# Kernel tuning notes

Measured on AMD Instinct MI355X. Metric: run time of the kernel, lower is better.

The kernel has to match this reference:

```python
import jax, jax.numpy as jnp
import numpy as np

HID, NH = 2048, 16
QLR, KVLR = 1536, 512
DR, DN, DQK, DV = 64, 128, 192, 128
S = 2048
EPS = 1e-06


def rmsnorm(x, w, eps=EPS):
    return x * jax.lax.rsqrt(jnp.mean(x * x, axis=-1, keepdims=True) + eps) * w


def rope_interleave(x, cos, sin):
    # x: [B,H,S,D]; cos/sin: [B,S,D] (unsqueezed to head dim 1)
    b, h, s, d = x.shape
    # DeepSeek-V3 interleave: (d//2, 2) -> transpose -> flatten
    x = x.reshape(b, h, s, d // 2, 2).swapaxes(3, 4).reshape(b, h, s, d)
    c = cos[:, None, :, :]
    sn = sin[:, None, :, :]
    x1, x2 = x[..., : d // 2], x[..., d // 2:]
    rot = jnp.concatenate([-x2, x1], axis=-1)
    return x * c + rot * sn


def setup_inputs() -> dict:
    key = jax.random.key(0)
    ks = jax.random.split(key, 8)
    hidden_states = jax.random.normal(ks[0], (1, S, HID), dtype=jnp.float32)
    # real RoPE tables for the 64-dim rope part
    inv_freq = 1.0 / (10000.0 ** (np.arange(0, DR, 2, dtype=np.float32) / DR))
    pos = np.arange(S, dtype=np.float32)
    freqs = pos[:, None] * inv_freq[None, :]          # [S, DR/2]
    emb = np.concatenate([freqs, freqs], axis=-1)     # [S, DR]
    cos = jnp.asarray(np.cos(emb), dtype=jnp.float32)[None]
    sin = jnp.asarray(np.sin(emb), dtype=jnp.float32)[None]
    w = 0.02
    wq_a = jax.random.normal(ks[1], (QLR, HID), dtype=jnp.float32) * w
    q_a_ln_w = jnp.ones((QLR,), dtype=jnp.float32)
    wq_b = jax.random.normal(ks[2], (NH * DQK, QLR), dtype=jnp.float32) * w
    wkv_a = jax.random.normal(ks[3], (KVLR + DR, HID), dtype=jnp.float32) * w
    kv_a_ln_w = jnp.ones((KVLR,), dtype=jnp.float32)
    wkv_b = jax.random.normal(ks[4], (NH * (DN + DV), KVLR), dtype=jnp.float32) * w
    wo = jax.random.normal(ks[5], (HID, NH * DV), dtype=jnp.float32) * w
    cu_seqlens = jnp.array([0, S // 2, S], dtype=jnp.int32)  # two packed docs
    return {"hidden_states": hidden_states, "cos": cos, "sin": sin,
            "wq_a": wq_a, "q_a_ln_w": q_a_ln_w, "wq_b": wq_b,
            "wkv_a": wkv_a, "kv_a_ln_w": kv_a_ln_w, "wkv_b": wkv_b,
            "wo": wo, "cu_seqlens": cu_seqlens, "max_seqlen": S // 2}


def reference(hidden_states, cos, sin, wq_a, q_a_ln_w, wq_b, wkv_a, kv_a_ln_w,
              wkv_b, wo, cu_seqlens, max_seqlen):
    B, s, _ = hidden_states.shape
    # LoRA-compressed Q: q_a -> RMSNorm -> q_b
    q = rmsnorm(hidden_states @ wq_a.T, q_a_ln_w) @ wq_b.T       # [B,S,NH*DQK]
    q = q.reshape(B, s, NH, DQK).transpose(0, 2, 1, 3)           # [B,NH,S,DQK]
    q_pass, q_rot = q[..., :DN], q[..., DN:]
    # compressed KV with MQA rope part
    ckv = hidden_states @ wkv_a.T                                 # [B,S,KVLR+DR]
    kv_c, k_rot = ckv[..., :KVLR], ckv[..., KVLR:]
    kv = rmsnorm(kv_c, kv_a_ln_w) @ wkv_b.T                       # [B,S,NH*(DN+DV)]
    kv = kv.reshape(B, s, NH, DN + DV).transpose(0, 2, 1, 3)      # [B,NH,S,DN+DV]
    k_pass, v = kv[..., :DN], kv[..., DN:]
    k_rot = k_rot[:, None, :, :]                                  # [B,1,S,DR]
    q_rot = rope_interleave(q_rot, cos, sin)
    k_rot = rope_interleave(k_rot, cos, sin)
    k_rot = jnp.broadcast_to(k_rot, (B, NH, s, DR))
    qf = jnp.concatenate([q_pass, q_rot], axis=-1)                # [B,NH,S,DQK]
    kf = jnp.concatenate([k_pass, k_rot], axis=-1)                # [B,NH,S,DQK]
    # varlen causal attention: block-diagonal per document + causal
    pos = jnp.arange(s)
    seg = jnp.searchsorted(cu_seqlens[1:], pos, side='right')
    mask = (seg[:, None] == seg[None, :]) & (pos[:, None] >= pos[None, :])
    scale = DQK ** -0.5  # flash default: 1/sqrt(q head dim) (v padded to DQK)
    scores = jnp.einsum('bhqd,bhkd->bhqk', qf, kf) * scale
    scores = jnp.where(mask[None, None], scores, jnp.finfo(scores.dtype).min)
    attn = jax.nn.softmax(scores, axis=-1)
    out = jnp.einsum('bhqk,bhkd->bhqd', attn, v)                  # [B,NH,S,DV]
    out = out.transpose(0, 2, 1, 3).reshape(B, s, NH * DV)
    return out @ wo.T
```

## Files before the change

### kernel.cpp

```cpp
#include <hip/hip_runtime.h>

typedef unsigned short u16;
typedef __attribute__((ext_vector_type(8))) short bf16x8;
typedef __attribute__((ext_vector_type(4))) float f32x4;

#define HID 2048
#define NH 16
#define QLR 1536
#define KVLR 512
#define DR 64
#define DN 128
#define DQK 192
#define DV 128
#define SEQ 2048
#define NKVA 2176
#define SCALE 0.07216878364870323f
#define SCL2 0.1041164359699839f
#define THR2 11.541560327111707f

static __device__ __forceinline__ u16 f2bf(float f) {
  unsigned v = __builtin_bit_cast(unsigned, f);
  v = v + 0x7fffu + ((v >> 16) & 1u);
  return (u16)(v >> 16);
}
static __device__ __forceinline__ float bf2f(u16 u) {
  unsigned v = ((unsigned)u) << 16;
  return __builtin_bit_cast(float, v);
}

#define GLOAD16(gp, lp)                                                        \
  __builtin_amdgcn_global_load_lds(                                            \
      (const __attribute__((address_space(1))) void*)(gp),                     \
      (__attribute__((address_space(3))) void*)(lp), 16, 0, 0)

__global__ void k_convert_all(const float* __restrict__ hs, const float* __restrict__ wq_a,
                              const float* __restrict__ wkv_a, const float* __restrict__ wqb,
                              const float* __restrict__ wkvb, const float* __restrict__ wo,
                              u16* __restrict__ hs_bf, u16* __restrict__ wqkva,
                              u16* __restrict__ wqb_bf, u16* __restrict__ wkvb_bf,
                              u16* __restrict__ wo_bf) {
  const long NQ = 4915200;
  long q = (long)blockIdx.x * blockDim.x + threadIdx.x;
  const long stride = (long)gridDim.x * blockDim.x;
  for (; q < NQ; q += stride) {
    const float* src;
    u16* dst;
    long li;
    bool zero = false;
    if (q < 1048576)        { src = hs;   dst = hs_bf;                      li = q; }
    else if (q < 1835008)   { src = wq_a; dst = wqkva;                      li = q - 1048576; }
    else if (q < 2162688)   { li = q - 1835008; src = wkv_a; dst = wqkva + (size_t)QLR * HID;
                              zero = (li >= 294912); }
    else if (q < 3342336)   { src = wqb;  dst = wqb_bf;                     li = q - 2162688; }
    else if (q < 3866624)   { src = wkvb; dst = wkvb_bf;                    li = q - 3342336; }
    else                    { src = wo;   dst = wo_bf;                      li = q - 3866624; }
    u16 o0 = 0, o1 = 0, o2 = 0, o3 = 0;
    if (!zero) {
      const float4 f = *(const float4*)(src + li * 4);
      o0 = f2bf(f.x); o1 = f2bf(f.y); o2 = f2bf(f.z); o3 = f2bf(f.w);
    }
    u16* d = dst + li * 4;
    d[0] = o0; d[1] = o1; d[2] = o2; d[3] = o3;
  }
}

__global__ void k_rmsnorm2(const float* __restrict__ qkva, const float* __restrict__ qw,
                           const float* __restrict__ kvw, u16* __restrict__ q_ln,
                           u16* __restrict__ kv_ln) {
  const int row = blockIdx.x;
  const int which = blockIdx.y;
  const int t = threadIdx.x;
  const int cols = which ? KVLR : QLR;
  const float inv_cols = which ? (1.0f / KVLR) : (1.0f / QLR);
  const float* x = qkva + (size_t)row * NKVA + (which ? QLR : 0);
  const float* w = which ? kvw : qw;
  u16* Y = (which ? kv_ln : q_ln) + (size_t)row * cols;
  float ss = 0.f;
  for (int i = t * 4; i < cols; i += 1024) {
    float4 v = *(const float4*)(x + i);
    ss += v.x * v.x + v.y * v.y + v.z * v.z + v.w * v.w;
  }
#pragma unroll
  for (int m = 1; m < 64; m <<= 1) ss += __shfl_xor(ss, m, 64);
  __shared__ float red[4];
  if ((t & 63) == 0) red[t >> 6] = ss;
  __syncthreads();
  float tot = red[0] + red[1] + red[2] + red[3];
  float r = rsqrtf(tot * inv_cols + 1e-6f);
  for (int i = t * 4; i < cols; i += 1024) {
    float4 v = *(const float4*)(x + i);
    float4 g = *(const float4*)(w + i);
    u16* y = Y + i;
    y[0] = f2bf(v.x * r * g.x);
    y[1] = f2bf(v.y * r * g.y);
    y[2] = f2bf(v.z * r * g.z);
    y[3] = f2bf(v.w * r * g.w);
  }
}

template <int WN, int NBUF>
__global__ __launch_bounds__(512) void k_gemm_nt8(
    const u16* __restrict__ A, const u16* __restrict__ B, void* __restrict__ Cout,
    int M, int N, int K, int mode) {
  constexpr int BN = WN * 64;
  constexpr int NST = 2 + WN;
  __shared__ __align__(16) u16 As[NBUF][128 * 64];
  __shared__ __align__(16) u16 Bs[NBUF][BN * 64];
  const int t = threadIdx.x;
  const int lane = t & 63;
  const int w = t >> 6, wr = w >> 2, wc = w & 3;
  const int lm = lane & 15, lg = lane >> 4;

  const int nwg = gridDim.x * gridDim.y;
  int bid = blockIdx.y * gridDim.x + blockIdx.x;
  if ((nwg & 7) == 0) bid = (bid & 7) * (nwg >> 3) + (bid >> 3);
  const int bm = bid % gridDim.y;
  const int bn = bid / gridDim.y;

  const u16* aT = A + (size_t)bm * 128 * K;
  const u16* bT = B + (size_t)bn * BN * K;

#define STAGE8(buf, kt_)                                                       \
  do {                                                                         \
    _Pragma("unroll") for (int i = 0; i < 2; ++i) {                            \
      const int g = t + i * 512, row = g >> 3, slot = (g & 7) ^ (row & 7);     \
      GLOAD16(aT + (size_t)row * K + slot * 8 + (kt_), (u16*)As[buf] + g * 8); \
    }                                                                          \
    _Pragma("unroll") for (int i = 0; i < WN; ++i) {                           \
      const int g = t + i * 512, row = g >> 3, slot = (g & 7) ^ (row & 7);     \
      GLOAD16(bT + (size_t)row * K + slot * 8 + (kt_), (u16*)Bs[buf] + g * 8); \
    }                                                                          \
  } while (0)

  f32x4 acc[4][WN] = {};
  const int nk = K >> 6;
#pragma unroll
  for (int b = 0; b < NBUF; ++b)
    if (b < nk) STAGE8(b, b << 6);
  int bt = 0;
  for (int kt = 0; kt < nk; ++kt) {
    const int rem = nk - 1 - kt;
    if constexpr (NBUF == 3) {
      if (rem >= 2)      asm volatile("s_waitcnt vmcnt(%0)" :: "i"(2 * NST) : "memory");
      else if (rem == 1) asm volatile("s_waitcnt vmcnt(%0)" :: "i"(NST) : "memory");
      else               asm volatile("s_waitcnt vmcnt(0)" ::: "memory");
    } else {
      if (rem >= 1)      asm volatile("s_waitcnt vmcnt(%0)" :: "i"(NST) : "memory");
      else               asm volatile("s_waitcnt vmcnt(0)" ::: "memory");
    }
    __builtin_amdgcn_s_barrier();
    __builtin_amdgcn_sched_barrier(0);
    bf16x8 af[2][4], bfr[2][WN];
#pragma unroll
    for (int kk = 0; kk < 2; ++kk) {
#pragma unroll
      for (int i = 0; i < 4; ++i) {
        const int row_ = wr * 64 + i * 16 + lm;
        af[kk][i] = *(const bf16x8*)(As[bt] + row_ * 64 +
                                     ((((kk << 2) | lg) ^ (row_ & 7)) << 3));
      }
#pragma unroll
      for (int j = 0; j < WN; ++j) {
        const int row_ = wc * (WN * 16) + j * 16 + lm;
        bfr[kk][j] = *(const bf16x8*)(Bs[bt] + row_ * 64 +
                                      ((((kk << 2) | lg) ^ (row_ & 7)) << 3));
      }
    }
    asm volatile("s_waitcnt lgkmcnt(0)" ::: "memory");
    __builtin_amdgcn_sched_barrier(0);
    __builtin_amdgcn_s_barrier();
    __builtin_amdgcn_sched_barrier(0);
    if (kt + NBUF < nk) STAGE8(bt, (kt + NBUF) << 6);
    __builtin_amdgcn_s_setprio(1);
#pragma unroll
    for (int kk = 0; kk < 2; ++kk)
#pragma unroll
      for (int i = 0; i < 4; ++i)
#pragma unroll
        for (int j = 0; j < WN; ++j)
          acc[i][j] = __builtin_amdgcn_mfma_f32_16x16x32_bf16(af[kk][i], bfr[kk][j],
                                                              acc[i][j], 0, 0, 0);
    __builtin_amdgcn_s_setprio(0);
    bt = (bt == NBUF - 1) ? 0 : bt + 1;
  }
#undef STAGE8

  const int row0 = bm * 128 + wr * 64 + lg * 4;
  const int col0 = bn * BN + wc * (WN * 16) + lm;
  if (mode == 1) {
    u16* C = (u16*)Cout;
#pragma unroll
    for (int i = 0; i < 4; ++i)
#pragma unroll
      for (int r = 0; r < 4; ++r) {
        u16* crow = C + (size_t)(row0 + i * 16 + r) * N + col0;
#pragma unroll
        for (int j = 0; j < WN; ++j) crow[j * 16] = f2bf(acc[i][j][r]);
      }
  } else {
    float* C = (float*)Cout;
#pragma unroll
    for (int i = 0; i < 4; ++i)
#pragma unroll
      for (int r = 0; r < 4; ++r) {
        float* crow = C + (size_t)(row0 + i * 16 + r) * N + col0;
#pragma unroll
        for (int j = 0; j < WN; ++j) crow[j * 16] = acc[i][j][r];
      }
  }
}

__global__ __launch_bounds__(256) void k_mk_all(
    const u16* __restrict__ qfull, const u16* __restrict__ kvfull,
    const float* __restrict__ krot, int krot_stride,
    const float* __restrict__ cosb, const float* __restrict__ sinb,
    u16* __restrict__ qf, u16* __restrict__ kf, u16* __restrict__ vt) {
  __shared__ u16 vts[128][66];
  const int s0 = blockIdx.x * 64, h = blockIdx.y, t = threadIdx.x;
#pragma unroll
  for (int i = 0; i < 8; ++i) {
    const int g = t + i * 256, row = g >> 5, slot = g & 31;
    const u16* src = kvfull + (size_t)(s0 + row) * (NH * 256) + h * 256 + slot * 8;
    bf16x8 v = *(const bf16x8*)src;
    if (slot < 16) {
      *(bf16x8*)(kf + ((size_t)h * SEQ + s0 + row) * DQK + slot * 8) = v;
    } else {
      const int d = (slot - 16) * 8;
#pragma unroll
      for (int e = 0; e < 8; ++e) vts[d + e][row] = (u16)v[e];
    }
  }
#pragma unroll
  for (int i = 0; i < 8; ++i) {
    const int g = t + i * 256, row = g >> 5, c = g & 31;
    const size_t kb = (size_t)(s0 + row) * krot_stride + 2 * c;
    float a = krot[kb];
    float b = krot[kb + 1];
    float cc = cosb[(size_t)(s0 + row) * DR + c];
    float sn = sinb[(size_t)(s0 + row) * DR + c];
    u16* kd = kf + ((size_t)h * SEQ + s0 + row) * DQK;
    kd[DN + c] = f2bf(a * cc - b * sn);
    kd[DN + 32 + c] = f2bf(b * cc + a * sn);
  }
  __syncthreads();
#pragma unroll
  for (int i = 0; i < 4; ++i) {
    const int g = t + i * 256, d = g >> 3, slot = g & 7;
    bf16x8 v;
#pragma unroll
    for (int e = 0; e < 8; ++e) v[e] = (short)vts[d][slot * 8 + e];
    *(bf16x8*)(vt + ((size_t)h * DV + d) * SEQ + s0 + slot * 8) = v;
  }
#pragma unroll
  for (int i = 0; i < 4; ++i) {
    const int g = t + i * 256, row = g >> 4, vc = g & 15;
    const u16* src = qfull + (size_t)(s0 + row) * (NH * DQK) + h * DQK + vc * 8;
    bf16x8 v = *(const bf16x8*)src;
    bf16x8 o;
#pragma unroll
    for (int e = 0; e < 8; ++e) o[e] = (short)f2bf(bf2f((u16)v[e]) * SCL2);
    *(bf16x8*)(qf + ((size_t)h * SEQ + s0 + row) * DQK + vc * 8) = o;
  }
#pragma unroll
  for (int i = 0; i < 8; ++i) {
    const int g = t + i * 256, row = g >> 5, c = g & 31;
    const u16* src = qfull + (size_t)(s0 + row) * (NH * DQK) + h * DQK;
    float a = bf2f(src[DN + 2 * c]);
    float b = bf2f(src[DN + 2 * c + 1]);
    float cc = cosb[(size_t)(s0 + row) * DR + c];
    float sn = sinb[(size_t)(s0 + row) * DR + c];
    u16* qd = qf + ((size_t)h * SEQ + s0 + row) * DQK;
    qd[DN + c] = f2bf((a * cc - b * sn) * SCL2);
    qd[DN + 32 + c] = f2bf((b * cc + a * sn) * SCL2);
  }
}

__global__ __launch_bounds__(256) void k_attn(
    const u16* __restrict__ qf, const u16* __restrict__ kf, const u16* __restrict__ vt,
    u16* __restrict__ attn_out, float* __restrict__ O_part, float* __restrict__ mlbuf) {
  __shared__ __align__(16) u16 Ks[2][32 * 192];
  __shared__ __align__(16) u16 Vs[2][128 * 32];
  __shared__ __align__(16) u16 p_lds[4][16][32];

  static const signed char TJ[24] = {15,15,7,14,14,13,13,6,12,12,11,11,5,
                                     10,10,9,9,4,8,8,3,2,1,0};
  static const signed char CK[24] = {0,1,2,0,1,0,1,2,0,1,0,1,2,
                                     0,1,0,1,2,0,1,2,2,2,2};

  const int t = threadIdx.x, lane = t & 63, w = t >> 6;
  const int lm = lane & 15, lg = lane >> 4;
  const int bid = blockIdx.x;
  const int x = bid & 7, rr = bid >> 3;
  const int hh = rr & 1, idx = rr >> 1;
  const int seg = idx & 1, slot = idx >> 1;
  const int tj = TJ[slot], ck = CK[slot];
  const int h = x * 2 + hh;
  const int tile_row0 = seg * 1024 + tj * 64;
  const int k_begin = seg * 1024;
  const int n_all = 2 * tj + 2;
  const int kt_lo = (ck == 1) ? (tj + 1) : 0;
  const int kt_hi = (ck == 0) ? (tj + 1) : n_all;
  const int n_kt = kt_hi - kt_lo;

  const int lo_row = tile_row0 + w * 16;
  bf16x8 qfr[6];
  {
    const u16* qp = qf + ((size_t)h * SEQ + (lo_row + lm)) * DQK + lg * 8;
#pragma unroll
    for (int c = 0; c < 6; ++c) qfr[c] = *(const bf16x8*)(qp + c * 32);
  }
  int qrow[4];
#pragma unroll
  for (int r = 0; r < 4; ++r) qrow[r] = lo_row + lg * 4 + r;

  float m_r[4], l_loc[4];
#pragma unroll
  for (int r = 0; r < 4; ++r) { m_r[r] = -3.0e4f; l_loc[r] = 0.f; }
  f32x4 oacc[8] = {};
  bf16x8 pa, vv[8];

#define STAGEA(buf, kt_)                                                       \
  do {                                                                         \
    const int k0_ = k_begin + (kt_) * 32;                                      \
    _Pragma("unroll") for (int p = 0; p < 3; ++p) {                            \
      const int id = p * 256 + t;                                              \
      const int row = id / 24, colL = id - row * 24;                           \
      const u16* g = kf + ((size_t)h * SEQ + k0_ + row) * DQK +                \
                     ((colL ^ (row & 7)) * 8);                                 \
      GLOAD16(g, (u16*)Ks[buf] + id * 8);                                      \
    }                                                                          \
    _Pragma("unroll") for (int p = 0; p < 2; ++p) {                            \
      const int id = p * 256 + t;                                              \
      const int row = id >> 2, colL = id & 3;                                  \
      const u16* g = vt + ((size_t)h * DV + row) * SEQ + k0_ +                 \
                     ((colL ^ (row & 3)) * 8);                                 \
      GLOAD16(g, (u16*)Vs[buf] + id * 8);                                      \
    }                                                                          \
  } while (0)

#define COMPUTE1(buf, kt_)                                                     \
  do {                                                                         \
    const int k0_ = k_begin + (kt_) * 32;                                      \
    f32x4 sc[2] = {};                                                          \
    __builtin_amdgcn_s_setprio(1);                                             \
    _Pragma("unroll") for (int n0_ = 0; n0_ < 2; ++n0_)                        \
        _Pragma("unroll") for (int c_ = 0; c_ < 6; ++c_) {                     \
      const int row_ = n0_ * 16 + lm, cc_ = c_ * 4 + lg;                       \
      bf16x8 kfr = *(const bf16x8*)(Ks[buf] + row_ * 192 +                     \
                                    ((cc_ ^ (row_ & 7)) * 8));                 \
      sc[n0_] = __builtin_amdgcn_mfma_f32_16x16x32_bf16(qfr[c_], kfr,          \
                                                        sc[n0_], 0, 0, 0);     \
    }                                                                          \
    __builtin_amdgcn_s_setprio(0);                                             \
    _Pragma("unroll") for (int nd = 0; nd < 8; ++nd) {                         \
      const int row_ = nd * 16 + lm;                                           \
      vv[nd] = *(const bf16x8*)(Vs[buf] + row_ * 32 +                          \
                                ((lg ^ (row_ & 3)) * 8));                      \
    }                                                                          \
    float s0a[4], s1a[4];                                                      \
    float over = -1e30f;                                                       \
    if (lo_row >= k0_ + 31) {                                                  \
      _Pragma("unroll") for (int r = 0; r < 4; ++r) {                          \
        s0a[r] = sc[0][r];                                                     \
        s1a[r] = sc[1][r];                                                     \
        over = fmaxf(over, fmaxf(s0a[r], s1a[r]) - m_r[r]);                    \
      }                                                                        \
    } else {                                                                   \
      const int kc0 = k0_ + lm, kc1 = k0_ + 16 + lm;                           \
      _Pragma("unroll") for (int r = 0; r < 4; ++r) {                          \
        s0a[r] = (kc0 <= qrow[r]) ? sc[0][r] : -1e30f;                         \
        s1a[r] = (kc1 <= qrow[r]) ? sc[1][r] : -1e30f;                         \
        over = fmaxf(over, fmaxf(s0a[r], s1a[r]) - m_r[r]);                    \
      }                                                                        \
    }                                                                          \
    if (__any(over > THR2)) {                                                  \
      _Pragma("unroll") for (int r = 0; r < 4; ++r) {                          \
        float mx = fmaxf(s0a[r], s1a[r]);                                      \
        _Pragma("unroll") for (int md = 1; md < 16; md <<= 1)                  \
            mx = fmaxf(mx, __shfl_xor(mx, md, 64));                            \
        float mnew = fmaxf(m_r[r], mx);                                        \
        float alpha = exp2f(m_r[r] - mnew);                                    \
        m_r[r] = mnew;                                                         \
        l_loc[r] *= alpha;                                                     \
        _Pragma("unroll") for (int nd = 0; nd < 8; ++nd) oacc[nd][r] *= alpha; \
      }                                                                        \
    }                                                                          \
    _Pragma("unroll") for (int r = 0; r < 4; ++r) {                            \
      float p0 = exp2f(s0a[r] - m_r[r]);                                       \
      float p1 = exp2f(s1a[r] - m_r[r]);                                       \
      l_loc[r] += p0 + p1;                                                     \
      p_lds[w][lg * 4 + r][lm] = f2bf(p0);                                     \
      p_lds[w][lg * 4 + r][16 + lm] = f2bf(p1);                                \
    }                                                                          \
    asm volatile("s_waitcnt lgkmcnt(0)" ::: "memory");                         \
    __builtin_amdgcn_sched_barrier(0);                                         \
    pa = *(const bf16x8*)(&p_lds[w][lm][lg * 8]);                              \
  } while (0)

  STAGEA(0, kt_lo);
  STAGEA(1, kt_lo + 1);
  for (int i = 0; i < n_kt; ++i) {
    const int kt = kt_lo + i;
    if (i + 1 < n_kt) asm volatile("s_waitcnt vmcnt(5)" ::: "memory");
    else              asm volatile("s_waitcnt vmcnt(0)" ::: "memory");
    __builtin_amdgcn_s_barrier();
    __builtin_amdgcn_sched_barrier(0);
    COMPUTE1(i & 1, kt);
    asm volatile("s_waitcnt lgkmcnt(0)" ::: "memory");
    __builtin_amdgcn_sched_barrier(0);
    __builtin_amdgcn_s_barrier();
    __builtin_amdgcn_sched_barrier(0);
    if (i + 2 < n_kt) STAGEA(i & 1, kt + 2);
    __builtin_amdgcn_s_setprio(1);
#pragma unroll
    for (int nd = 0; nd < 8; ++nd)
      oacc[nd] = __builtin_amdgcn_mfma_f32_16x16x32_bf16(pa, vv[nd], oacc[nd], 0, 0, 0);
    __builtin_amdgcn_s_setprio(0);
  }
#undef STAGEA
#undef COMPUTE1

  float l_row[4];
#pragma unroll
  for (int r = 0; r < 4; ++r) {
    float lt = l_loc[r];
#pragma unroll
    for (int md = 1; md < 16; md <<= 1) lt += __shfl_xor(lt, md, 64);
    l_row[r] = lt;
  }

  if (ck == 2) {
#pragma unroll
    for (int r = 0; r < 4; ++r) {
      float inv = 1.0f / l_row[r];
#pragma unroll
      for (int nd = 0; nd < 8; ++nd)
        attn_out[(size_t)qrow[r] * (NH * DV) + h * DV + nd * 16 + lm] =
            f2bf(oacc[nd][r] * inv);
    }
  } else {
    const int part = (((tj - 8) * 2 + seg) * 16 + h) * 2 + ck;
    float* op = O_part + (size_t)part * 8192;
#pragma unroll
    for (int r = 0; r < 4; ++r) {
      const int rw = w * 16 + lg * 4 + r;
#pragma unroll
      for (int nd = 0; nd < 8; ++nd)
        op[rw * 128 + nd * 16 + lm] = oacc[nd][r];
      if (lm == 0) {
        mlbuf[part * 128 + rw] = m_r[r];
        mlbuf[part * 128 + 64 + rw] = l_row[r];
      }
    }
  }
}

__global__ __launch_bounds__(256) void k_merge(const float* __restrict__ O_part,
                                               const float* __restrict__ mlbuf,
                                               u16* __restrict__ attn_out) {
  const int b = blockIdx.x;
  const int h = b & 15, z = b >> 4;
  const int tj = 8 + (z >> 1), seg = z & 1;
  const int p0 = (((tj - 8) * 2 + seg) * 16 + h) * 2;
  const int p1 = p0 + 1;
  const int t = threadIdx.x;
  const int row = t >> 2, cg = t & 3;

  const float m0 = mlbuf[p0 * 128 + row], l0 = mlbuf[p0 * 128 + 64 + row];
  const float m1 = mlbuf[p1 * 128 + row], l1 = mlbuf[p1 * 128 + 64 + row];
  const float M = fmaxf(m0, m1);
  const float w0 = exp2f(m0 - M), w1 = exp2f(m1 - M);
  const float inv = 1.0f / (w0 * l0 + w1 * l1);
  const float a0 = w0 * inv, a1 = w1 * inv;

  const int qrow = seg * 1024 + tj * 64 + row;
  const float* o0 = O_part + (size_t)p0 * 8192 + row * 128 + cg * 32;
  const float* o1 = O_part + (size_t)p1 * 8192 + row * 128 + cg * 32;
  u16* dst = attn_out + (size_t)qrow * (NH * DV) + h * DV + cg * 32;
#pragma unroll
  for (int e = 0; e < 32; e += 4) {
    const float4 u = *(const float4*)(o0 + e);
    const float4 v = *(const float4*)(o1 + e);
    dst[e]     = f2bf(a0 * u.x + a1 * v.x);
    dst[e + 1] = f2bf(a0 * u.y + a1 * v.y);
    dst[e + 2] = f2bf(a0 * u.z + a1 * v.z);
    dst[e + 3] = f2bf(a0 * u.w + a1 * v.w);
  }
}

extern "C" void kernel_launch(void* const* d_in, const int* in_sizes, int n_in,
                              void* d_out, int out_size, void* d_ws, size_t ws_size,
                              hipStream_t stream) {
  const float* hs = (const float*)d_in[0];
  const float* cosb = (const float*)d_in[1];
  const float* sinb = (const float*)d_in[2];
  const float* wq_a = (const float*)d_in[3];
  const float* q_a_ln_w = (const float*)d_in[4];
  const float* wq_b = (const float*)d_in[5];
  const float* wkv_a = (const float*)d_in[6];
  const float* kv_a_ln_w = (const float*)d_in[7];
  const float* wkv_b = (const float*)d_in[8];
  const float* wo = (const float*)d_in[9];

  char* ws = (char*)d_ws;
  size_t off = 0;
  auto take = [&](size_t bytes) {
    size_t o = off;
    off += (bytes + 255) & ~(size_t)255;
    return o;
  };
  u16* hs_bf = (u16*)(ws + take((size_t)SEQ * HID * 2));
  u16* wqkva = (u16*)(ws + take((size_t)NKVA * HID * 2));
  u16* wqb = (u16*)(ws + take((size_t)(NH * DQK) * QLR * 2));
  u16* wkvb = (u16*)(ws + take((size_t)(NH * 256) * KVLR * 2));
  u16* wo_bf = (u16*)(ws + take((size_t)HID * (NH * DV) * 2));
  float* qkva = (float*)(ws + take((size_t)SEQ * NKVA * 4));
  u16* q_ln = (u16*)(ws + take((size_t)SEQ * QLR * 2));
  u16* kv_ln = (u16*)(ws + take((size_t)SEQ * KVLR * 2));
  u16* qfull = (u16*)(ws + take((size_t)SEQ * NH * DQK * 2));
  u16* kvfull = (u16*)(ws + take((size_t)SEQ * NH * 256 * 2));
  u16* qf = (u16*)(ws + take((size_t)NH * SEQ * DQK * 2));
  u16* kf = (u16*)(ws + take((size_t)NH * SEQ * DQK * 2));
  u16* vt = (u16*)(ws + take((size_t)NH * DV * SEQ * 2));
  u16* attn = (u16*)(ws + take((size_t)SEQ * NH * DV * 2));
  if (off > ws_size) return;
  float* O_part = (float*)kvfull;
  float* mlbuf = (float*)qfull;

  k_convert_all<<<2048, 256, 0, stream>>>(hs, wq_a, wkv_a, wq_b, wkv_b, wo,
                                          hs_bf, wqkva, wqb, wkvb, wo_bf);

  dim3 g1(NKVA / 128, SEQ / 128);
  k_gemm_nt8<2, 2><<<g1, 512, 0, stream>>>(hs_bf, wqkva, qkva, SEQ, NKVA, HID, 0);

  k_rmsnorm2<<<dim3(SEQ, 2), 256, 0, stream>>>(qkva, q_a_ln_w, kv_a_ln_w, q_ln, kv_ln);

  dim3 g2(NH * DQK / 192, SEQ / 128);
  k_gemm_nt8<3, 2><<<g2, 512, 0, stream>>>(q_ln, wqb, qfull, SEQ, NH * DQK, QLR, 1);
  dim3 g3(NH * 256 / 256, SEQ / 128);
  k_gemm_nt8<4, 2><<<g3, 512, 0, stream>>>(kv_ln, wkvb, kvfull, SEQ, NH * 256, KVLR, 1);

  k_mk_all<<<dim3(SEQ / 64, NH), 256, 0, stream>>>(qfull, kvfull, qkva + (QLR + KVLR),
                                                   NKVA, cosb, sinb, qf, kf, vt);

  k_attn<<<768, 256, 0, stream>>>(qf, kf, vt, attn, O_part, mlbuf);
  k_merge<<<256, 256, 0, stream>>>(O_part, mlbuf, attn);

  dim3 g4(HID / 128, SEQ / 128);
  k_gemm_nt8<2, 2><<<g4, 512, 0, stream>>>(attn, wo_bf, d_out, SEQ, HID, NH * DV, 0);
}
```

Before: 183.5 us.

## Fuse Q RoPE/scale and K/V split-transpose into GEMM epilogues

```diff
diff --git a/kernel.cpp b/kernel.cpp
--- a/kernel.cpp
+++ b/kernel.cpp
@@ -98,14 +98,16 @@
   }
 }
 
-template <int WN, int NBUF>
+template <int WN, int NBUF, int MODE>
 __global__ __launch_bounds__(512) void k_gemm_nt8(
     const u16* __restrict__ A, const u16* __restrict__ B, void* __restrict__ Cout,
-    int M, int N, int K, int mode) {
+    int M, int N, int K, const float* __restrict__ cosb, const float* __restrict__ sinb,
+    u16* __restrict__ out_a, u16* __restrict__ out_b) {
   constexpr int BN = WN * 64;
   constexpr int NST = 2 + WN;
   __shared__ __align__(16) u16 As[NBUF][128 * 64];
   __shared__ __align__(16) u16 Bs[NBUF][BN * 64];
+  __shared__ __align__(16) u16 vts[MODE == 3 ? 128 * 130 : 2];
   const int t = threadIdx.x;
   const int lane = t & 63;
   const int w = t >> 6, wr = w >> 2, wc = w & 3;
@@ -187,7 +189,7 @@
 
   const int row0 = bm * 128 + wr * 64 + lg * 4;
   const int col0 = bn * BN + wc * (WN * 16) + lm;
-  if (mode == 1) {
+  if constexpr (MODE == 1) {
     u16* C = (u16*)Cout;
 #pragma unroll
     for (int i = 0; i < 4; ++i)
@@ -197,7 +199,7 @@
 #pragma unroll
         for (int j = 0; j < WN; ++j) crow[j * 16] = f2bf(acc[i][j][r]);
       }
-  } else {
+  } else if constexpr (MODE == 0) {
     float* C = (float*)Cout;
 #pragma unroll
     for (int i = 0; i < 4; ++i)
@@ -207,72 +209,80 @@
 #pragma unroll
         for (int j = 0; j < WN; ++j) crow[j * 16] = acc[i][j][r];
       }
-  }
-}
-
-__global__ __launch_bounds__(256) void k_mk_all(
-    const u16* __restrict__ qfull, const u16* __restrict__ kvfull,
-    const float* __restrict__ krot, int krot_stride,
-    const float* __restrict__ cosb, const float* __restrict__ sinb,
-    u16* __restrict__ qf, u16* __restrict__ kf, u16* __restrict__ vt) {
-  __shared__ u16 vts[128][66];
-  const int s0 = blockIdx.x * 64, h = blockIdx.y, t = threadIdx.x;
-#pragma unroll
-  for (int i = 0; i < 8; ++i) {
-    const int g = t + i * 256, row = g >> 5, slot = g & 31;
-    const u16* src = kvfull + (size_t)(s0 + row) * (NH * 256) + h * 256 + slot * 8;
-    bf16x8 v = *(const bf16x8*)src;
-    if (slot < 16) {
-      *(bf16x8*)(kf + ((size_t)h * SEQ + s0 + row) * DQK + slot * 8) = v;
-    } else {
-      const int d = (slot - 16) * 8;
-#pragma unroll
-      for (int e = 0; e < 8; ++e) vts[d + e][row] = (u16)v[e];
+  } else if constexpr (MODE == 2) {
+    const int h = bn;
+#pragma unroll
+    for (int i = 0; i < 4; ++i)
+#pragma unroll
+      for (int r = 0; r < 4; ++r) {
+        const int s = row0 + i * 16 + r;
+        u16* qrow = out_a + ((size_t)h * SEQ + s) * DQK;
+#pragma unroll
+        for (int j = 0; j < WN; ++j) {
+          const int c = wc * 48 + j * 16 + lm;
+          float val = acc[i][j][r];
+          float partner = __shfl_xor(val, 1, 64);
+          if (c < 128) {
+            qrow[c] = f2bf(val * SCL2);
+          } else {
+            const int u = c - 128, p = u >> 1, od = u & 1;
+            float cv = cosb[(size_t)s * DR + p];
+            float sv = sinb[(size_t)s * DR + p];
+            float o = od ? (val * cv + partner * sv) : (val * cv - partner * sv);
+            qrow[128 + od * 32 + p] = f2bf(o * SCL2);
+          }
+        }
+      }
+  } else {
+    const int h = bn;
+    const int sl0 = wr * 64 + lg * 4;
+#pragma unroll
+    for (int i = 0; i < 4; ++i)
+#pragma unroll
+      for (int r = 0; r < 4; ++r) {
+        const int s = row0 + i * 16 + r;
+        const int sl = sl0 + i * 16 + r;
+#pragma unroll
+        for (int j = 0; j < WN; ++j) {
+          const int c = wc * 64 + j * 16 + lm;
+          const u16 bv = f2bf(acc[i][j][r]);
+          if (c < 128) out_a[((size_t)h * SEQ + s) * DQK + c] = bv;
+          else vts[(c - 128) * 130 + sl] = bv;
+        }
+      }
+    __syncthreads();
+    const int d = t >> 2, q4 = t & 3;
+#pragma unroll
+    for (int sub = 0; sub < 4; ++sub) {
+      bf16x8 v;
+#pragma unroll
+      for (int e = 0; e < 8; ++e) v[e] = (short)vts[d * 130 + q4 * 32 + sub * 8 + e];
+      *(bf16x8*)(out_b + ((size_t)h * DV + d) * SEQ + bm * 128 + q4 * 32 + sub * 8) = v;
     }
   }
-#pragma unroll
-  for (int i = 0; i < 8; ++i) {
-    const int g = t + i * 256, row = g >> 5, c = g & 31;
-    const size_t kb = (size_t)(s0 + row) * krot_stride + 2 * c;
-    float a = krot[kb];
-    float b = krot[kb + 1];
-    float cc = cosb[(size_t)(s0 + row) * DR + c];
-    float sn = sinb[(size_t)(s0 + row) * DR + c];
-    u16* kd = kf + ((size_t)h * SEQ + s0 + row) * DQK;
-    kd[DN + c] = f2bf(a * cc - b * sn);
-    kd[DN + 32 + c] = f2bf(b * cc + a * sn);
-  }
-  __syncthreads();
-#pragma unroll
-  for (int i = 0; i < 4; ++i) {
-    const int g = t + i * 256, d = g >> 3, slot = g & 7;
-    bf16x8 v;
-#pragma unroll
-    for (int e = 0; e < 8; ++e) v[e] = (short)vts[d][slot * 8 + e];
-    *(bf16x8*)(vt + ((size_t)h * DV + d) * SEQ + s0 + slot * 8) = v;
-  }
-#pragma unroll
-  for (int i = 0; i < 4; ++i) {
-    const int g = t + i * 256, row = g >> 4, vc = g & 15;
-    const u16* src = qfull + (size_t)(s0 + row) * (NH * DQK) + h * DQK + vc * 8;
-    bf16x8 v = *(const bf16x8*)src;
-    bf16x8 o;
-#pragma unroll
-    for (int e = 0; e < 8; ++e) o[e] = (short)f2bf(bf2f((u16)v[e]) * SCL2);
-    *(bf16x8*)(qf + ((size_t)h * SEQ + s0 + row) * DQK + vc * 8) = o;
-  }
-#pragma unroll
-  for (int i = 0; i < 8; ++i) {
-    const int g = t + i * 256, row = g >> 5, c = g & 31;
-    const u16* src = qfull + (size_t)(s0 + row) * (NH * DQK) + h * DQK;
-    float a = bf2f(src[DN + 2 * c]);
-    float b = bf2f(src[DN + 2 * c + 1]);
-    float cc = cosb[(size_t)(s0 + row) * DR + c];
-    float sn = sinb[(size_t)(s0 + row) * DR + c];
-    u16* qd = qf + ((size_t)h * SEQ + s0 + row) * DQK;
-    qd[DN + c] = f2bf((a * cc - b * sn) * SCL2);
-    qd[DN + 32 + c] = f2bf((b * cc + a * sn) * SCL2);
-  }
+}
+
+__global__ __launch_bounds__(256) void k_rope_k(
+    const float* __restrict__ krot, int stride, const float* __restrict__ cosb,
+    const float* __restrict__ sinb, u16* __restrict__ kf) {
+  const int s0 = blockIdx.x * 32;
+  const int t = threadIdx.x;
+  const int row = t >> 3, c8 = t & 7;
+  const int s = s0 + row;
+  const int half = c8 >> 2, p0 = (c8 & 3) * 8;
+  bf16x8 v;
+#pragma unroll
+  for (int e = 0; e < 8; ++e) {
+    const int p = p0 + e;
+    float a = krot[(size_t)s * stride + 2 * p];
+    float b = krot[(size_t)s * stride + 2 * p + 1];
+    float cv = cosb[(size_t)s * DR + p];
+    float sv = sinb[(size_t)s * DR + p];
+    v[e] = (short)f2bf(half ? (b * cv + a * sv) : (a * cv - b * sv));
+  }
+#pragma unroll
+  for (int h = 0; h < NH; ++h)
+    *(bf16x8*)(kf + ((size_t)h * SEQ + s) * DQK + 128 + half * 32 + p0) = v;
 }
 
 __global__ __launch_bounds__(256) void k_attn(
@@ -517,35 +527,36 @@
   float* qkva = (float*)(ws + take((size_t)SEQ * NKVA * 4));
   u16* q_ln = (u16*)(ws + take((size_t)SEQ * QLR * 2));
   u16* kv_ln = (u16*)(ws + take((size_t)SEQ * KVLR * 2));
-  u16* qfull = (u16*)(ws + take((size_t)SEQ * NH * DQK * 2));
-  u16* kvfull = (u16*)(ws + take((size_t)SEQ * NH * 256 * 2));
   u16* qf = (u16*)(ws + take((size_t)NH * SEQ * DQK * 2));
   u16* kf = (u16*)(ws + take((size_t)NH * SEQ * DQK * 2));
   u16* vt = (u16*)(ws + take((size_t)NH * DV * SEQ * 2));
   u16* attn = (u16*)(ws + take((size_t)SEQ * NH * DV * 2));
+  float* O_part = (float*)(ws + take((size_t)512 * 8192 * 4));
+  float* mlbuf = (float*)(ws + take((size_t)512 * 128 * 4));
   if (off > ws_size) return;
-  float* O_part = (float*)kvfull;
-  float* mlbuf = (float*)qfull;
 
   k_convert_all<<<2048, 256, 0, stream>>>(hs, wq_a, wkv_a, wq_b, wkv_b, wo,
                                           hs_bf, wqkva, wqb, wkvb, wo_bf);
 
   dim3 g1(NKVA / 128, SEQ / 128);
-  k_gemm_nt8<2, 2><<<g1, 512, 0, stream>>>(hs_bf, wqkva, qkva, SEQ, NKVA, HID, 0);
+  k_gemm_nt8<2, 2, 0><<<g1, 512, 0, stream>>>(hs_bf, wqkva, qkva, SEQ, NKVA, HID,
+                                              nullptr, nullptr, nullptr, nullptr);
 
   k_rmsnorm2<<<dim3(SEQ, 2), 256, 0, stream>>>(qkva, q_a_ln_w, kv_a_ln_w, q_ln, kv_ln);
 
+  k_rope_k<<<SEQ / 32, 256, 0, stream>>>(qkva + (QLR + KVLR), NKVA, cosb, sinb, kf);
+
   dim3 g2(NH * DQK / 192, SEQ / 128);
-  k_gemm_nt8<3, 2><<<g2, 512, 0, stream>>>(q_ln, wqb, qfull, SEQ, NH * DQK, QLR, 1);
+  k_gemm_nt8<3, 2, 2><<<g2, 512, 0, stream>>>(q_ln, wqb, nullptr, SEQ, NH * DQK, QLR,
+                                              cosb, sinb, qf, nullptr);
   dim3 g3(NH * 256 / 256, SEQ / 128);
-  k_gemm_nt8<4, 2><<<g3, 512, 0, stream>>>(kv_ln, wkvb, kvfull, SEQ, NH * 256, KVLR, 1);
-
-  k_mk_all<<<dim3(SEQ / 64, NH), 256, 0, stream>>>(qfull, kvfull, qkva + (QLR + KVLR),
-                                                   NKVA, cosb, sinb, qf, kf, vt);
+  k_gemm_nt8<4, 2, 3><<<g3, 512, 0, stream>>>(kv_ln, wkvb, nullptr, SEQ, NH * 256, KVLR,
+                                              nullptr, nullptr, kf, vt);
 
   k_attn<<<768, 256, 0, stream>>>(qf, kf, vt, attn, O_part, mlbuf);
   k_merge<<<256, 256, 0, stream>>>(O_part, mlbuf, attn);
 
   dim3 g4(HID / 128, SEQ / 128);
-  k_gemm_nt8<2, 2><<<g4, 512, 0, stream>>>(attn, wo_bf, d_out, SEQ, HID, NH * DV, 0);
-}
+  k_gemm_nt8<2, 2, 0><<<g4, 512, 0, stream>>>(attn, wo_bf, d_out, SEQ, HID, NH * DV,
+                                              nullptr, nullptr, nullptr, nullptr);
+}
```

Result: no change. 184.4 us (+0.5%).
